# Performance work log

Hardware: AMD Instinct MI355X
Metric: run time of the kernel (lower is better)

## Reference

```python
import jax, jax.numpy as jnp
import numpy as np

P = 0.5  # dropout probability (mask precomputed as rand < P)

def setup_inputs() -> dict:
    key = jax.random.key(0)
    kx, km = jax.random.split(key)
    B, C, T, F, K = 32, 16, 512, 256, 128
    X = jax.random.normal(kx, (B, C, T, F), dtype=jnp.float32)
    idx = jnp.arange(K, dtype=jnp.int32) * 2  # even feature channels, in-range [0, F)
    mask = jax.random.uniform(km, (B, C, T, K)) < P  # True -> dropped
    return {"X": X, "idx": idx, "mask": mask}

def reference(X, idx, mask):
    # Gather the included channels: [B, C, T, K]
    sub = X[..., idx]
    K = sub.shape[-1]
    # Total 'power' per row before dropout: [B, C, T]
    power = jnp.sum(sub, axis=-1)
    # Binary dropout: zero where mask is True
    zeroed = jnp.where(mask, jnp.float32(0), sub)
    # Sum compensation: redistribute the dropped mass uniformly over K channels.
    # (Equivalent to the original repeat + Fortran-reshape broadcast.)
    comp = (power - jnp.sum(zeroed, axis=-1)) / K  # [B, C, T]
    new_sub = zeroed + comp[..., None]
    # Scatter back into the full tensor
    return X.at[..., idx].set(new_sub)
```

## Files before the change

kernel.cpp:

```cpp
#include <hip/hip_runtime.h>
#include <stdint.h>


__global__ __launch_bounds__(256) void dropout_partial_kernel(
    const float* __restrict__ X,
    const int* __restrict__ mask,
    float* __restrict__ out,
    int nrows)
{
    const int wave = threadIdx.x >> 6;
    const int lane = threadIdx.x & 63;
    const int row  = blockIdx.x * 4 + wave;
    if (row >= nrows) return;

    const float4* __restrict__ xrow = (const float4*)(X + (size_t)row * 256);
    float4*       __restrict__ orow = (float4*)(out + (size_t)row * 256);
    const int2*   __restrict__ mrow = (const int2*)(mask + (size_t)row * 128);

    float4 x = xrow[lane];
    int2   m = mrow[lane];

    float dropped = (m.x ? x.x : 0.0f) + (m.y ? x.z : 0.0f);

    #pragma unroll
    for (int off = 32; off > 0; off >>= 1)
        dropped += __shfl_xor(dropped, off, 64);

    const float comp = dropped * (1.0f / 128.0f);

    float4 o;
    o.x = (m.x ? 0.0f : x.x) + comp;
    o.y = x.y;
    o.z = (m.y ? 0.0f : x.z) + comp;
    o.w = x.w;
    orow[lane] = o;
}

extern "C" void kernel_launch(void* const* d_in, const int* in_sizes, int n_in,
                              void* d_out, int out_size, void* d_ws, size_t ws_size,
                              hipStream_t stream) {
    const float* X    = (const float*)d_in[0];
    const int*   mask = (const int*)d_in[2];
    float*       out  = (float*)d_out;

    const int nrows = in_sizes[0] / 256;
    dim3 grid((nrows + 3) / 4), block(256);
    hipLaunchKernelGGL(dropout_partial_kernel, grid, block, 0, stream,
                       X, mask, out, nrows);
}
```

Baseline: 494.2 us.

## Process two rows per wave with grid-stride loop and wider loads

Each wave now handles two rows at a time, one per half-wave, with each lane loading two float4 of X and one int4 of mask. The launch is a fixed grid of up to 2048 blocks that walks the rows with a grid-stride loop. The aim is more bytes in flight per lane, a shorter shuffle reduction and less block launch overhead. It assumes an even row count and the mask stored as int32, and the fixed grid may leave the device underoccupied for memory latency hiding.

```diff
diff --git a/kernel.cpp b/kernel.cpp
--- a/kernel.cpp
+++ b/kernel.cpp
@@ -6,34 +6,42 @@
     const float* __restrict__ X,
     const int* __restrict__ mask,
     float* __restrict__ out,
-    int nrows)
+    int nrowpairs)
 {
-    const int wave = threadIdx.x >> 6;
-    const int lane = threadIdx.x & 63;
-    const int row  = blockIdx.x * 4 + wave;
-    if (row >= nrows) return;
+    const int wid    = blockIdx.x * 4 + (threadIdx.x >> 6);
+    const int lane   = threadIdx.x & 63;
+    const int half   = lane >> 5;
+    const int l      = lane & 31;
+    const int nwaves = gridDim.x * 4;
 
-    const float4* __restrict__ xrow = (const float4*)(X + (size_t)row * 256);
-    float4*       __restrict__ orow = (float4*)(out + (size_t)row * 256);
-    const int2*   __restrict__ mrow = (const int2*)(mask + (size_t)row * 128);
+    #pragma unroll 2
+    for (int wp = wid; wp < nrowpairs; wp += nwaves) {
+        const size_t row = (size_t)wp * 2 + half;
+        const float4* __restrict__ xrow = (const float4*)(X   + row * 256) + (l << 1);
+        float4*       __restrict__ orow = (float4*)      (out + row * 256) + (l << 1);
+        const int4*   __restrict__ mrow = (const int4*)  (mask + row * 128) + l;
 
-    float4 x = xrow[lane];
-    int2   m = mrow[lane];
+        float4 a0 = xrow[0];
+        float4 a1 = xrow[1];
+        int4   m  = *mrow;
 
-    float dropped = (m.x ? x.x : 0.0f) + (m.y ? x.z : 0.0f);
+        float dropped = (m.x ? a0.x : 0.0f) + (m.y ? a0.z : 0.0f)
+                      + (m.z ? a1.x : 0.0f) + (m.w ? a1.z : 0.0f);
 
-    #pragma unroll
-    for (int off = 32; off > 0; off >>= 1)
-        dropped += __shfl_xor(dropped, off, 64);
+        #pragma unroll
+        for (int off = 16; off > 0; off >>= 1)
+            dropped += __shfl_xor(dropped, off, 64);
 
-    const float comp = dropped * (1.0f / 128.0f);
+        const float comp = dropped * (1.0f / 128.0f);
 
-    float4 o;
-    o.x = (m.x ? 0.0f : x.x) + comp;
-    o.y = x.y;
-    o.z = (m.y ? 0.0f : x.z) + comp;
-    o.w = x.w;
-    orow[lane] = o;
+        float4 o0, o1;
+        o0.x = (m.x ? 0.0f : a0.x) + comp;  o0.y = a0.y;
+        o0.z = (m.y ? 0.0f : a0.z) + comp;  o0.w = a0.w;
+        o1.x = (m.z ? 0.0f : a1.x) + comp;  o1.y = a1.y;
+        o1.z = (m.w ? 0.0f : a1.z) + comp;  o1.w = a1.w;
+        orow[0] = o0;
+        orow[1] = o1;
+    }
 }
 
 extern "C" void kernel_launch(void* const* d_in, const int* in_sizes, int n_in,
@@ -43,8 +51,13 @@
     const int*   mask = (const int*)d_in[2];
     float*       out  = (float*)d_out;
 
-    const int nrows = in_sizes[0] / 256;
-    dim3 grid((nrows + 3) / 4), block(256);
+    const int nrows     = in_sizes[0] / 256;
+    const int nrowpairs = nrows >> 1;
+
+    int blocks = 2048;
+    if (blocks * 4 > nrowpairs) blocks = (nrowpairs + 3) / 4;
+
+    dim3 grid(blocks), block(256);
     hipLaunchKernelGGL(dropout_partial_kernel, grid, block, 0, stream,
-                       X, mask, out, nrows);
+                       X, mask, out, nrowpairs);
 }
```

Result: slower. 510.1 us (+3.2%).

## Use persistent grid-stride loop with prefetch, DPP reduction, and nontemporal access

Applied to the files above, without the earlier changes.

Replaces the one-row-per-wave launch with a fixed grid of persistent waves that each process two rows per iteration and prefetch the next pair before computing the current one. The cross-lane sum now uses DPP row shifts and broadcasts with a readlane instead of shuffle-xor. Mask loads and output stores are marked nontemporal. The goal is more memory-level parallelism and less cache pollution in a bandwidth-bound kernel, at the cost of extra registers and a fixed grid size that may not saturate all CUs.

```diff
diff --git a/kernel.cpp b/kernel.cpp
--- a/kernel.cpp
+++ b/kernel.cpp
@@ -2,38 +2,77 @@
 #include <stdint.h>
 
 
+typedef float f32x4 __attribute__((ext_vector_type(4)));
+typedef int   i32x2 __attribute__((ext_vector_type(2)));
+
+template<int CTRL>
+__device__ __forceinline__ float dpp_add(float acc) {
+    int s = __builtin_amdgcn_update_dpp(0, __float_as_int(acc), CTRL, 0xF, 0xF, false);
+    return acc + __int_as_float(s);
+}
+
+__device__ __forceinline__ float wave_sum64(float v) {
+    v = dpp_add<0x111>(v);
+    v = dpp_add<0x112>(v);
+    v = dpp_add<0x114>(v);
+    v = dpp_add<0x118>(v);
+    v = dpp_add<0x142>(v);
+    v = dpp_add<0x143>(v);
+    return __int_as_float(__builtin_amdgcn_readlane(__float_as_int(v), 63));
+}
+
 __global__ __launch_bounds__(256) void dropout_partial_kernel(
     const float* __restrict__ X,
-    const int* __restrict__ mask,
-    float* __restrict__ out,
+    const int*   __restrict__ mask,
+    float*       __restrict__ out,
     int nrows)
 {
-    const int wave = threadIdx.x >> 6;
-    const int lane = threadIdx.x & 63;
-    const int row  = blockIdx.x * 4 + wave;
-    if (row >= nrows) return;
+    const int wid    = (blockIdx.x << 2) + (threadIdx.x >> 6);
+    const int lane   = threadIdx.x & 63;
+    const int stride = gridDim.x << 3;
 
-    const float4* __restrict__ xrow = (const float4*)(X + (size_t)row * 256);
-    float4*       __restrict__ orow = (float4*)(out + (size_t)row * 256);
-    const int2*   __restrict__ mrow = (const int2*)(mask + (size_t)row * 128);
+    const f32x4* __restrict__ xv = (const f32x4*)X;
+    const i32x2* __restrict__ mv = (const i32x2*)mask;
+    f32x4*       __restrict__ ov = (f32x4*)out;
 
-    float4 x = xrow[lane];
-    int2   m = mrow[lane];
+    int r = wid << 1;
+    if (r >= nrows) return;
 
-    float dropped = (m.x ? x.x : 0.0f) + (m.y ? x.z : 0.0f);
+    f32x4 xa0 = xv[(size_t)r * 64 + lane];
+    f32x4 xa1 = xv[(size_t)(r + 1) * 64 + lane];
+    i32x2 ma0 = __builtin_nontemporal_load(mv + (size_t)r * 64 + lane);
+    i32x2 ma1 = __builtin_nontemporal_load(mv + (size_t)(r + 1) * 64 + lane);
 
-    #pragma unroll
-    for (int off = 32; off > 0; off >>= 1)
-        dropped += __shfl_xor(dropped, off, 64);
+    while (true) {
+        const int  rn   = r + stride;
+        const bool next = (rn < nrows);
 
-    const float comp = dropped * (1.0f / 128.0f);
+        f32x4 xb0, xb1; i32x2 mb0, mb1;
+        if (next) {
+            xb0 = xv[(size_t)rn * 64 + lane];
+            xb1 = xv[(size_t)(rn + 1) * 64 + lane];
+            mb0 = __builtin_nontemporal_load(mv + (size_t)rn * 64 + lane);
+            mb1 = __builtin_nontemporal_load(mv + (size_t)(rn + 1) * 64 + lane);
+        }
 
-    float4 o;
-    o.x = (m.x ? 0.0f : x.x) + comp;
-    o.y = x.y;
-    o.z = (m.y ? 0.0f : x.z) + comp;
-    o.w = x.w;
-    orow[lane] = o;
+        float d0 = (ma0.x ? xa0.x : 0.0f) + (ma0.y ? xa0.z : 0.0f);
+        float d1 = (ma1.x ? xa1.x : 0.0f) + (ma1.y ? xa1.z : 0.0f);
+        float c0 = wave_sum64(d0) * (1.0f / 128.0f);
+        float c1 = wave_sum64(d1) * (1.0f / 128.0f);
+
+        f32x4 o0, o1;
+        o0.x = (ma0.x ? 0.0f : xa0.x) + c0;  o0.y = xa0.y;
+        o0.z = (ma0.y ? 0.0f : xa0.z) + c0;  o0.w = xa0.w;
+        o1.x = (ma1.x ? 0.0f : xa1.x) + c1;  o1.y = xa1.y;
+        o1.z = (ma1.y ? 0.0f : xa1.z) + c1;  o1.w = xa1.w;
+
+        __builtin_nontemporal_store(o0, ov + (size_t)r * 64 + lane);
+        __builtin_nontemporal_store(o1, ov + (size_t)(r + 1) * 64 + lane);
+
+        if (!next) break;
+        r = rn;
+        xa0 = xb0; xa1 = xb1; ma0 = mb0; ma1 = mb1;
+    }
 }
 
 extern "C" void kernel_launch(void* const* d_in, const int* in_sizes, int n_in,
@@ -44,7 +83,12 @@
     float*       out  = (float*)d_out;
 
     const int nrows = in_sizes[0] / 256;
-    dim3 grid((nrows + 3) / 4), block(256);
+
+    int blocks = 2048;
+    const int maxb = (nrows + 7) / 8;
+    if (blocks > maxb) blocks = maxb;
+
+    dim3 grid(blocks), block(256);
     hipLaunchKernelGGL(dropout_partial_kernel, grid, block, 0, stream,
                        X, mask, out, nrows);
 }
```

Result: slower. 524.2 us (+6.1%).
